# Kernel tuning notes

Hardware: AMD Instinct MI355X
Metric: run time of the kernel (lower is better)

The kernel has to match this reference:

```python
import jax, jax.numpy as jnp
import numpy as np

B, S, D, H = 4, 2048, 1024, 16
HD = D // H  # head dim = 64


def setup_inputs() -> dict:
    key = jax.random.key(0)
    ks = jax.random.split(key, 5)
    scale = 1.0 / np.sqrt(D)
    return {
        "X": jax.random.normal(ks[0], (B, S, D), dtype=jnp.float32),
        "Wq": jax.random.normal(ks[1], (D, D), dtype=jnp.float32) * scale,
        "Wk": jax.random.normal(ks[2], (D, D), dtype=jnp.float32) * scale,
        "Wv": jax.random.normal(ks[3], (D, D), dtype=jnp.float32) * scale,
        "Wo": jax.random.normal(ks[4], (D, D), dtype=jnp.float32) * scale,
    }


def _split_heads(x):
    # [B, S, D] -> [B, H, S, HD]
    b, s, d = x.shape
    return x.reshape(b, s, H, HD).transpose(0, 2, 1, 3)


def reference(X, Wq, Wk, Wv, Wo):
    q = _split_heads(X @ Wq)  # [B, H, S, HD]
    k = _split_heads(X @ Wk)
    v = _split_heads(X @ Wv)
    scores = jnp.einsum("bhqd,bhkd->bhqk", q, k) / jnp.sqrt(jnp.float32(HD))
    causal = jnp.tril(jnp.ones((S, S), dtype=bool))  # [S, S]
    scores = jnp.where(causal[None, None, :, :], scores, jnp.float32(-jnp.inf))
    attn = jax.nn.softmax(scores, axis=-1)
    out = jnp.einsum("bhqk,bhkd->bhqd", attn, v)  # [B, H, S, HD]
    out = out.transpose(0, 2, 1, 3).reshape(B, S, D)  # merge heads
    return out @ Wo
```

## Files before the change

### kernel.cpp

```cpp
#include <hip/hip_runtime.h>
#include <hip/hip_bf16.h>

typedef __attribute__((ext_vector_type(8))) short short8;
typedef __attribute__((ext_vector_type(8))) unsigned short ushort8;
typedef __attribute__((ext_vector_type(4))) unsigned short bf16x4;
typedef __attribute__((ext_vector_type(4))) float f32x4;

#define BDIM 1024
#define SEQ  2048
#define NHD  16
#define NEGBIG (-1.0e30f)

__device__ __forceinline__ unsigned short f2bf(float x) {
  union { __hip_bfloat16 h; unsigned short u; } cv;
  cv.h = __float2bfloat16(x);
  return cv.u;
}

__device__ __forceinline__ void gload16(const void* g, void* l) {
  __builtin_amdgcn_global_load_lds((const __attribute__((address_space(1))) void*)g,
                                   (__attribute__((address_space(3))) void*)l, 16, 0, 0);
}

__global__ __launch_bounds__(256) void cvt_f32_bf16(const float* __restrict__ src,
                                                    unsigned short* __restrict__ dst) {
  int i = (blockIdx.x * 256 + threadIdx.x) * 8;
  float4 a = *(const float4*)(src + i);
  float4 b = *(const float4*)(src + i + 4);
  ushort8 o;
  o[0] = f2bf(a.x); o[1] = f2bf(a.y); o[2] = f2bf(a.z); o[3] = f2bf(a.w);
  o[4] = f2bf(b.x); o[5] = f2bf(b.y); o[6] = f2bf(b.z); o[7] = f2bf(b.w);
  *(ushort8*)(dst + i) = o;
}

__global__ __launch_bounds__(256) void wtrans4(const float* __restrict__ s0, const float* __restrict__ s1,
                                               const float* __restrict__ s2, const float* __restrict__ s3,
                                               unsigned short* __restrict__ d0, unsigned short* __restrict__ d1,
                                               unsigned short* __restrict__ d2, unsigned short* __restrict__ d3) {
  const float* src = blockIdx.z == 0 ? s0 : blockIdx.z == 1 ? s1 : blockIdx.z == 2 ? s2 : s3;
  unsigned short* dst = blockIdx.z == 0 ? d0 : blockIdx.z == 1 ? d1 : blockIdx.z == 2 ? d2 : d3;
  __shared__ float t[32][33];
  int tx = threadIdx.x, ty = threadIdx.y;
  int c0 = blockIdx.x * 32, r0 = blockIdx.y * 32;
  for (int i = ty; i < 32; i += 8)
    t[i][tx] = src[(size_t)(r0 + i) * BDIM + c0 + tx];
  __syncthreads();
  for (int i = ty; i < 32; i += 8)
    dst[(size_t)(c0 + i) * BDIM + r0 + tx] = f2bf(t[tx][i]);
}

template <bool F32OUT>
__device__ __forceinline__ void gemm_body(const unsigned short* __restrict__ A,
                                          const unsigned short* __restrict__ BT,
                                          void* __restrict__ Cv,
                                          unsigned short* As, unsigned short* Bs) {
  const int tid = threadIdx.x;
  const int lane = tid & 63;
  const int w = tid >> 6;
  const int wr = w >> 1, wc = w & 1;
  const int m0 = blockIdx.x * 128;
  const int n0 = blockIdx.y * 128;
  const int l15 = lane & 15, lg = lane >> 4;

  int ob[4], grow[4], gcol[4];
  for (int j = 0; j < 4; ++j) {
    ob[j] = (w * 4 + j) * 1024;
    int o = ob[j] + lane * 16;
    int row = o >> 7;
    int kb = (o & 127) ^ ((row & 7) << 4);
    grow[j] = row; gcol[j] = kb >> 1;
  }

  f32x4 acc[4][4] = {};

  for (int j = 0; j < 4; ++j) {
    gload16(A + (size_t)(m0 + grow[j]) * BDIM + gcol[j], (char*)As + ob[j]);
    gload16(BT + (size_t)(n0 + grow[j]) * BDIM + gcol[j], (char*)Bs + ob[j]);
  }
  __syncthreads();

  int cur = 0;
  for (int k0 = 0; k0 < BDIM; k0 += 64) {
    if (k0 + 64 < BDIM) {
      int nb = (cur ^ 1) * 16384;
      for (int j = 0; j < 4; ++j) {
        gload16(A + (size_t)(m0 + grow[j]) * BDIM + (k0 + 64) + gcol[j], (char*)As + nb + ob[j]);
        gload16(BT + (size_t)(n0 + grow[j]) * BDIM + (k0 + 64) + gcol[j], (char*)Bs + nb + ob[j]);
      }
    }
    const char* Ab = (const char*)As + cur * 16384;
    const char* Bb = (const char*)Bs + cur * 16384;
    for (int ks = 0; ks < 64; ks += 32) {
      int kb = (ks + lg * 8) * 2;
      short8 a[4], b[4];
      for (int mi = 0; mi < 4; ++mi) {
        int row = wr * 64 + mi * 16 + l15;
        a[mi] = *(const short8*)(Ab + row * 128 + (kb ^ ((row & 7) << 4)));
      }
      for (int nj = 0; nj < 4; ++nj) {
        int row = wc * 64 + nj * 16 + l15;
        b[nj] = *(const short8*)(Bb + row * 128 + (kb ^ ((row & 7) << 4)));
      }
      for (int mi = 0; mi < 4; ++mi)
        for (int nj = 0; nj < 4; ++nj)
          acc[mi][nj] = __builtin_amdgcn_mfma_f32_16x16x32_bf16(a[mi], b[nj], acc[mi][nj], 0, 0, 0);
    }
    __syncthreads();
    cur ^= 1;
  }

  for (int mi = 0; mi < 4; ++mi)
    for (int nj = 0; nj < 4; ++nj) {
      int m = m0 + wr * 64 + mi * 16 + lg * 4;
      int n = n0 + wc * 64 + nj * 16 + l15;
      for (int r = 0; r < 4; ++r) {
        if constexpr (F32OUT)
          ((float*)Cv)[(size_t)(m + r) * BDIM + n] = acc[mi][nj][r];
        else
          ((unsigned short*)Cv)[(size_t)(m + r) * BDIM + n] = f2bf(acc[mi][nj][r]);
      }
    }
}

__global__ __launch_bounds__(256) void gemm_qkv(const unsigned short* __restrict__ A,
                                                const unsigned short* __restrict__ B0,
                                                const unsigned short* __restrict__ B1,
                                                const unsigned short* __restrict__ B2,
                                                unsigned short* __restrict__ C0,
                                                unsigned short* __restrict__ C1,
                                                unsigned short* __restrict__ C2) {
  __shared__ __align__(16) unsigned short As[2 * 128 * 64];
  __shared__ __align__(16) unsigned short Bs[2 * 128 * 64];
  const unsigned short* BT = blockIdx.z == 0 ? B0 : blockIdx.z == 1 ? B1 : B2;
  unsigned short* C = blockIdx.z == 0 ? C0 : blockIdx.z == 1 ? C1 : C2;
  gemm_body<false>(A, BT, C, As, Bs);
}

template <bool F32OUT>
__global__ __launch_bounds__(256) void gemm_bt(const unsigned short* __restrict__ A,
                                               const unsigned short* __restrict__ BT,
                                               void* __restrict__ Cv) {
  __shared__ __align__(16) unsigned short As[2 * 128 * 64];
  __shared__ __align__(16) unsigned short Bs[2 * 128 * 64];
  gemm_body<F32OUT>(A, BT, Cv, As, Bs);
}

__global__ __launch_bounds__(512) void attn(const unsigned short* __restrict__ Qg,
                                            const unsigned short* __restrict__ Kg,
                                            const unsigned short* __restrict__ Vg,
                                            unsigned short* __restrict__ Og) {
  __shared__ __align__(16) unsigned short Ks[2][64 * 64];
  __shared__ __align__(16) unsigned short VTs[2][64 * 64];
  __shared__ __align__(16) unsigned short Ps[128 * 64];

  const int tid = threadIdx.x;
  const int lane = tid & 63;
  const int w = tid >> 6;
  const int l15 = lane & 15, lg = lane >> 4;
  const int bh = blockIdx.x;
  const size_t base = ((size_t)(bh >> 4) * SEQ) * BDIM + (size_t)(bh & 15) * 64;
  constexpr float C = 0.125f * 1.44269504089f;

  const int srow = tid >> 3;
  const int scol = (((tid & 7) * 16) ^ ((srow & 7) << 4)) >> 1;
  const int sdst = tid * 16;
  const int vp = tid & 31, vd = tid >> 5;
  int vdst[4];
  for (int e = 0; e < 4; ++e) {
    int d = vd * 4 + e;
    vdst[e] = d * 128 + ((4 * vp) ^ ((((d & 7) ^ (d >> 3)) & 7) << 4));
  }

  const int c = 15 - (int)blockIdx.y;
  const int q0 = c * 128;

  gload16(Qg + base + (size_t)(q0 + srow) * BDIM + scol, (char*)Ps + sdst);
  gload16(Qg + base + (size_t)(q0 + 64 + srow) * BDIM + scol, (char*)Ps + 8192 + sdst);
  __syncthreads();
  short8 qf[2];
  {
    int row = w * 16 + l15;
    int sz = (row & 7) << 4;
    qf[0] = *(const short8*)((const char*)Ps + row * 128 + ((lg * 16) ^ sz));
    qf[1] = *(const short8*)((const char*)Ps + row * 128 + ((64 + lg * 16) ^ sz));
  }

  float mrow = NEGBIG, lrow = 0.f;
  f32x4 oacc[4] = {};

  const int ntiles = 2 * c + 2;

  bf16x4 v0, v1;
  gload16(Kg + base + (size_t)(srow) * BDIM + scol, (char*)Ks[0] + sdst);
  {
    const unsigned short* vs = Vg + base + (size_t)(2 * vp) * BDIM + vd * 4;
    v0 = *(const bf16x4*)vs;
    v1 = *(const bf16x4*)(vs + BDIM);
  }
  for (int e = 0; e < 4; ++e) {
    unsigned int pk = (unsigned int)v0[e] | ((unsigned int)v1[e] << 16);
    *(unsigned int*)((char*)VTs[0] + vdst[e]) = pk;
  }
  __syncthreads();

  int cur = 0;
  for (int t = 0; t < ntiles; ++t) {
    const int kv0 = t * 64;
    const bool more = (t + 1 < ntiles);
    if (more) {
      const int nv0 = kv0 + 64;
      gload16(Kg + base + (size_t)(nv0 + srow) * BDIM + scol, (char*)Ks[cur ^ 1] + sdst);
      const unsigned short* vs = Vg + base + (size_t)(nv0 + 2 * vp) * BDIM + vd * 4;
      v0 = *(const bf16x4*)vs;
      v1 = *(const bf16x4*)(vs + BDIM);
    }

    if (kv0 <= q0 + w * 16 + 15) {
      f32x4 s2[4];
      __builtin_amdgcn_s_setprio(1);
      for (int kvj = 0; kvj < 4; ++kvj) {
        int row = kvj * 16 + l15;
        int sz = (row & 7) << 4;
        short8 kf0 = *(const short8*)((const char*)Ks[cur] + row * 128 + ((lg * 16) ^ sz));
        short8 kf1 = *(const short8*)((const char*)Ks[cur] + row * 128 + ((64 + lg * 16) ^ sz));
        f32x4 z = {};
        z = __builtin_amdgcn_mfma_f32_16x16x32_bf16(kf0, qf[0], z, 0, 0, 0);
        z = __builtin_amdgcn_mfma_f32_16x16x32_bf16(kf1, qf[1], z, 0, 0, 0);
        s2[kvj] = z;
      }
      __builtin_amdgcn_s_setprio(0);
      const int qbase = q0 + w * 16;
      const int qc = qbase + l15;
      float mx = NEGBIG;
      if (kv0 + 63 > qbase) {
        for (int kvj = 0; kvj < 4; ++kvj)
          for (int r = 0; r < 4; ++r) {
            int kv = kv0 + kvj * 16 + 4 * lg + r;
            float v = s2[kvj][r];
            if (kv > qc) { v = NEGBIG; s2[kvj][r] = v; }
            mx = fmaxf(mx, v);
          }
      } else {
        for (int kvj = 0; kvj < 4; ++kvj)
          for (int r = 0; r < 4; ++r) mx = fmaxf(mx, s2[kvj][r]);
      }
      mx = fmaxf(mx, __shfl_xor(mx, 16));
      mx = fmaxf(mx, __shfl_xor(mx, 32));
      if (!__all(mx <= mrow)) {
        float mnew = fmaxf(mrow, mx);
        float sc = __builtin_amdgcn_exp2f((mrow - mnew) * C);
        mrow = mnew;
        lrow *= sc;
        for (int di = 0; di < 4; ++di)
          for (int r = 0; r < 4; ++r) oacc[di][r] *= sc;
      }
      const float mC = mrow * C;
      float rs = 0.f;
      for (int kvj = 0; kvj < 4; ++kvj)
        for (int r = 0; r < 4; ++r) {
          float p = __builtin_amdgcn_exp2f(fmaf(s2[kvj][r], C, -mC));
          s2[kvj][r] = p;
          rs += p;
        }
      rs += __shfl_xor(rs, 16);
      rs += __shfl_xor(rs, 32);
      lrow += rs;
      int prow = w * 16 + l15;
      int psz = (prow & 7) << 4;
      for (int kvj = 0; kvj < 4; ++kvj) {
        bf16x4 pk;
        pk[0] = f2bf(s2[kvj][0]); pk[1] = f2bf(s2[kvj][1]);
        pk[2] = f2bf(s2[kvj][2]); pk[3] = f2bf(s2[kvj][3]);
        *(bf16x4*)((char*)Ps + prow * 128 + ((kvj * 32 + lg * 8) ^ psz)) = pk;
      }
      __builtin_amdgcn_s_setprio(1);
      for (int ks = 0; ks < 2; ++ks) {
        short8 pa = *(const short8*)((const char*)Ps + prow * 128 +
                                     ((ks * 64 + lg * 16) ^ psz));
        for (int di = 0; di < 4; ++di) {
          int d = di * 16 + l15;
          short8 vf = *(const short8*)((const char*)VTs[cur] + d * 128 +
                                       ((ks * 64 + lg * 16) ^ ((((d & 7) ^ (d >> 3)) & 7) << 4)));
          oacc[di] = __builtin_amdgcn_mfma_f32_16x16x32_bf16(vf, pa, oacc[di], 0, 0, 0);
        }
      }
      __builtin_amdgcn_s_setprio(0);
    }

    if (more) {
      for (int e = 0; e < 4; ++e) {
        unsigned int pk = (unsigned int)v0[e] | ((unsigned int)v1[e] << 16);
        *(unsigned int*)((char*)VTs[cur ^ 1] + vdst[e]) = pk;
      }
    }
    __syncthreads();
    cur ^= 1;
  }

  {
    float inv = 1.0f / lrow;
    int qrow = q0 + w * 16 + l15;
    for (int di = 0; di < 4; ++di) {
      bf16x4 ov;
      for (int r = 0; r < 4; ++r) ov[r] = f2bf(oacc[di][r] * inv);
      *(bf16x4*)(Og + base + (size_t)qrow * BDIM + di * 16 + 4 * lg) = ov;
    }
  }
}

extern "C" void kernel_launch(void* const* d_in, const int* in_sizes, int n_in,
                              void* d_out, int out_size, void* d_ws, size_t ws_size,
                              hipStream_t stream) {
  const float* X  = (const float*)d_in[0];
  const float* Wq = (const float*)d_in[1];
  const float* Wk = (const float*)d_in[2];
  const float* Wv = (const float*)d_in[3];
  const float* Wo = (const float*)d_in[4];

  const size_t WSZ = (size_t)1024 * 1024;
  const size_t MSZ = (size_t)8192 * 1024;
  const size_t need = (4 * WSZ + 4 * MSZ) * 2;
  if (ws_size < need) return;

  unsigned short* ws = (unsigned short*)d_ws;
  unsigned short* WqT = ws;
  unsigned short* WkT = WqT + WSZ;
  unsigned short* WvT = WkT + WSZ;
  unsigned short* WoT = WvT + WSZ;
  unsigned short* Qw  = WoT + WSZ;
  unsigned short* Kw  = Qw + MSZ;
  unsigned short* Vw  = Kw + MSZ;
  unsigned short* Ow  = Vw + MSZ;
  unsigned short* Xb  = (unsigned short*)d_out;

  wtrans4<<<dim3(32, 32, 4), dim3(32, 8), 0, stream>>>(Wq, Wk, Wv, Wo, WqT, WkT, WvT, WoT);

  cvt_f32_bf16<<<(8192 * 1024) / (256 * 8), 256, 0, stream>>>(X, Xb);

  gemm_qkv<<<dim3(64, 8, 3), 256, 0, stream>>>(Xb, WqT, WkT, WvT, Qw, Kw, Vw);

  attn<<<dim3(64, 16), 512, 0, stream>>>(Qw, Kw, Vw, Ow);

  gemm_bt<true><<<dim3(64, 8), 256, 0, stream>>>(Ow, WoT, d_out);
}
```

Baseline: 169.3 us.

## Single-buffer attention K/V tiles and merge the prep kernels into one launch

The attention kernel drops double-buffered K and V^T shared-memory tiles in favour of single buffers. It adds an extra barrier so the next K tile is prefetched only after the QK^T MFMAs have read the current one, and V^T is rewritten only after the PV product. This cuts LDS per block from 48KB to 32KB, which may allow more resident blocks per CU, at the cost of an extra __syncthreads per tile and less overlap between loads and compute. Separately, the weight-transpose and X conversion kernels are fused into a single launch using extra z-slices of the grid, saving one kernel launch.

```diff
diff --git a/kernel.cpp b/kernel.cpp
--- a/kernel.cpp
+++ b/kernel.cpp
@@ -22,23 +22,25 @@
                                    (__attribute__((address_space(3))) void*)l, 16, 0, 0);
 }
 
-__global__ __launch_bounds__(256) void cvt_f32_bf16(const float* __restrict__ src,
-                                                    unsigned short* __restrict__ dst) {
-  int i = (blockIdx.x * 256 + threadIdx.x) * 8;
-  float4 a = *(const float4*)(src + i);
-  float4 b = *(const float4*)(src + i + 4);
-  ushort8 o;
-  o[0] = f2bf(a.x); o[1] = f2bf(a.y); o[2] = f2bf(a.z); o[3] = f2bf(a.w);
-  o[4] = f2bf(b.x); o[5] = f2bf(b.y); o[6] = f2bf(b.z); o[7] = f2bf(b.w);
-  *(ushort8*)(dst + i) = o;
-}
-
-__global__ __launch_bounds__(256) void wtrans4(const float* __restrict__ s0, const float* __restrict__ s1,
-                                               const float* __restrict__ s2, const float* __restrict__ s3,
-                                               unsigned short* __restrict__ d0, unsigned short* __restrict__ d1,
-                                               unsigned short* __restrict__ d2, unsigned short* __restrict__ d3) {
-  const float* src = blockIdx.z == 0 ? s0 : blockIdx.z == 1 ? s1 : blockIdx.z == 2 ? s2 : s3;
-  unsigned short* dst = blockIdx.z == 0 ? d0 : blockIdx.z == 1 ? d1 : blockIdx.z == 2 ? d2 : d3;
+__global__ __launch_bounds__(256) void prep(const float* __restrict__ X, unsigned short* __restrict__ Xb,
+                                            const float* __restrict__ s0, const float* __restrict__ s1,
+                                            const float* __restrict__ s2, const float* __restrict__ s3,
+                                            unsigned short* __restrict__ d0, unsigned short* __restrict__ d1,
+                                            unsigned short* __restrict__ d2, unsigned short* __restrict__ d3) {
+  const int z = blockIdx.z;
+  const int tid = threadIdx.y * 32 + threadIdx.x;
+  if (z >= 4) {
+    int i = (((z - 4) * 1024 + blockIdx.y * 32 + blockIdx.x) * 256 + tid) * 8;
+    float4 a = *(const float4*)(X + i);
+    float4 b = *(const float4*)(X + i + 4);
+    ushort8 o;
+    o[0] = f2bf(a.x); o[1] = f2bf(a.y); o[2] = f2bf(a.z); o[3] = f2bf(a.w);
+    o[4] = f2bf(b.x); o[5] = f2bf(b.y); o[6] = f2bf(b.z); o[7] = f2bf(b.w);
+    *(ushort8*)(Xb + i) = o;
+    return;
+  }
+  const float* src = z == 0 ? s0 : z == 1 ? s1 : z == 2 ? s2 : s3;
+  unsigned short* dst = z == 0 ? d0 : z == 1 ? d1 : z == 2 ? d2 : d3;
   __shared__ float t[32][33];
   int tx = threadIdx.x, ty = threadIdx.y;
   int c0 = blockIdx.x * 32, r0 = blockIdx.y * 32;
@@ -149,8 +151,8 @@
                                             const unsigned short* __restrict__ Kg,
                                             const unsigned short* __restrict__ Vg,
                                             unsigned short* __restrict__ Og) {
-  __shared__ __align__(16) unsigned short Ks[2][64 * 64];
-  __shared__ __align__(16) unsigned short VTs[2][64 * 64];
+  __shared__ __align__(16) unsigned short Ks[64 * 64];
+  __shared__ __align__(16) unsigned short VTs[64 * 64];
   __shared__ __align__(16) unsigned short Ps[128 * 64];
 
   const int tid = threadIdx.x;
@@ -191,7 +193,7 @@
   const int ntiles = 2 * c + 2;
 
   bf16x4 v0, v1;
-  gload16(Kg + base + (size_t)(srow) * BDIM + scol, (char*)Ks[0] + sdst);
+  gload16(Kg + base + (size_t)(srow) * BDIM + scol, (char*)Ks + sdst);
   {
     const unsigned short* vs = Vg + base + (size_t)(2 * vp) * BDIM + vd * 4;
     v0 = *(const bf16x4*)vs;
@@ -199,36 +201,42 @@
   }
   for (int e = 0; e < 4; ++e) {
     unsigned int pk = (unsigned int)v0[e] | ((unsigned int)v1[e] << 16);
-    *(unsigned int*)((char*)VTs[0] + vdst[e]) = pk;
+    *(unsigned int*)((char*)VTs + vdst[e]) = pk;
   }
   __syncthreads();
 
-  int cur = 0;
   for (int t = 0; t < ntiles; ++t) {
     const int kv0 = t * 64;
     const bool more = (t + 1 < ntiles);
+    const bool live = kv0 <= q0 + w * 16 + 15;
+
     if (more) {
-      const int nv0 = kv0 + 64;
-      gload16(Kg + base + (size_t)(nv0 + srow) * BDIM + scol, (char*)Ks[cur ^ 1] + sdst);
-      const unsigned short* vs = Vg + base + (size_t)(nv0 + 2 * vp) * BDIM + vd * 4;
+      const unsigned short* vs = Vg + base + (size_t)(kv0 + 64 + 2 * vp) * BDIM + vd * 4;
       v0 = *(const bf16x4*)vs;
       v1 = *(const bf16x4*)(vs + BDIM);
     }
 
-    if (kv0 <= q0 + w * 16 + 15) {
-      f32x4 s2[4];
+    f32x4 s2[4];
+    if (live) {
       __builtin_amdgcn_s_setprio(1);
       for (int kvj = 0; kvj < 4; ++kvj) {
         int row = kvj * 16 + l15;
         int sz = (row & 7) << 4;
-        short8 kf0 = *(const short8*)((const char*)Ks[cur] + row * 128 + ((lg * 16) ^ sz));
-        short8 kf1 = *(const short8*)((const char*)Ks[cur] + row * 128 + ((64 + lg * 16) ^ sz));
+        short8 kf0 = *(const short8*)((const char*)Ks + row * 128 + ((lg * 16) ^ sz));
+        short8 kf1 = *(const short8*)((const char*)Ks + row * 128 + ((64 + lg * 16) ^ sz));
         f32x4 z = {};
         z = __builtin_amdgcn_mfma_f32_16x16x32_bf16(kf0, qf[0], z, 0, 0, 0);
         z = __builtin_amdgcn_mfma_f32_16x16x32_bf16(kf1, qf[1], z, 0, 0, 0);
         s2[kvj] = z;
       }
       __builtin_amdgcn_s_setprio(0);
+    }
+    __syncthreads();
+
+    if (more)
+      gload16(Kg + base + (size_t)(kv0 + 64 + srow) * BDIM + scol, (char*)Ks + sdst);
+
+    if (live) {
       const int qbase = q0 + w * 16;
       const int qc = qbase + l15;
       float mx = NEGBIG;
@@ -279,22 +287,21 @@
                                      ((ks * 64 + lg * 16) ^ psz));
         for (int di = 0; di < 4; ++di) {
           int d = di * 16 + l15;
-          short8 vf = *(const short8*)((const char*)VTs[cur] + d * 128 +
+          short8 vf = *(const short8*)((const char*)VTs + d * 128 +
                                        ((ks * 64 + lg * 16) ^ ((((d & 7) ^ (d >> 3)) & 7) << 4)));
           oacc[di] = __builtin_amdgcn_mfma_f32_16x16x32_bf16(vf, pa, oacc[di], 0, 0, 0);
         }
       }
       __builtin_amdgcn_s_setprio(0);
     }
+    __syncthreads();
 
     if (more) {
       for (int e = 0; e < 4; ++e) {
         unsigned int pk = (unsigned int)v0[e] | ((unsigned int)v1[e] << 16);
-        *(unsigned int*)((char*)VTs[cur ^ 1] + vdst[e]) = pk;
-      }
-    }
-    __syncthreads();
-    cur ^= 1;
+        *(unsigned int*)((char*)VTs + vdst[e]) = pk;
+      }
+    }
   }
 
   {
@@ -333,9 +340,7 @@
   unsigned short* Ow  = Vw + MSZ;
   unsigned short* Xb  = (unsigned short*)d_out;
 
-  wtrans4<<<dim3(32, 32, 4), dim3(32, 8), 0, stream>>>(Wq, Wk, Wv, Wo, WqT, WkT, WvT, WoT);
-
-  cvt_f32_bf16<<<(8192 * 1024) / (256 * 8), 256, 0, stream>>>(X, Xb);
+  prep<<<dim3(32, 32, 8), dim3(32, 8), 0, stream>>>(X, Xb, Wq, Wk, Wv, Wo, WqT, WkT, WvT, WoT);
 
   gemm_qkv<<<dim3(64, 8, 3), 256, 0, stream>>>(Xb, WqT, WkT, WvT, Qw, Kw, Vw);
 
```

Result: no change. 169.1 us (-0.1%).
